# Kernel optimization log

Hardware: AMD Instinct MI355X
Metric: run time of the kernel (lower is better)

## Reference

```python
import jax, jax.numpy as jnp
import numpy as np

LN_EPS = 1e-12


def setup_inputs() -> dict:
    key = jax.random.key(0)
    k1, k2, k3, k4 = jax.random.split(key, 4)
    B, H, L, D = 2, 12, 2048, 64
    q = jax.random.normal(k1, (B, H, L, D), dtype=jnp.float32)
    k = jax.random.normal(k2, (B, H, L, D), dtype=jnp.float32)
    v = jax.random.normal(k3, (B, H, L, D), dtype=jnp.float32)
    mask = jax.random.randint(k4, (1, 1, L, L), 0, 2).astype(jnp.int32)
    gamma = jnp.ones((D,), dtype=jnp.float32)
    beta = jnp.zeros((D,), dtype=jnp.float32)
    return {"q": q, "k": k, "v": v, "mask": mask, "gamma": gamma, "beta": beta}


def reference(q, k, v, mask, gamma, beta):
    # score = q @ k^T  -> [B, H, L, L]
    score = jnp.einsum("bhqd,bhkd->bhqk", q, k)
    # masked_fill(mask == 0, -10000)
    score = jnp.where(mask == 0, jnp.float32(-10000.0), score)
    # result = score @ v -> [B, H, L, D]  (no softmax)
    result = jnp.einsum("bhqk,bhkd->bhqd", score, v)
    # layer norm over the last dim (d_tensor)
    mean = jnp.mean(result, axis=-1, keepdims=True)
    var = jnp.var(result, axis=-1, keepdims=True)
    normed = (result - mean) / jnp.sqrt(var + LN_EPS)
    return normed * gamma + beta
```

## Files before the change

kernel.cpp:

```cpp
#include <hip/hip_runtime.h>

#define SEQ 2048
#define HD 64
#define NBH 24
#define ROWB 144

#define MB_OFF   0
#define MB_BYTES (32 * 32 * 512)
#define QB_OFF   (MB_OFF + MB_BYTES)
#define QK_BYTES (NBH * SEQ * HD * 2)
#define KB_OFF   (QB_OFF + QK_BYTES)
#define VT_OFF   (KB_OFF + QK_BYTES)
#define WS_NEED  ((size_t)(VT_OFF + QK_BYTES))

typedef __bf16 bfrag8 __attribute__((ext_vector_type(8)));
typedef __bf16 bf16x4 __attribute__((ext_vector_type(4)));
typedef float  floatx4 __attribute__((ext_vector_type(4)));

__device__ __forceinline__ floatx4 mfma_16x16x32(bfrag8 a, bfrag8 b, floatx4 c) {
    return __builtin_amdgcn_mfma_f32_16x16x32_bf16(a, b, c, 0, 0, 0);
}

__global__ __launch_bounds__(256)
void prep_kernel(const float* __restrict__ qp, const float* __restrict__ kp,
                 const float* __restrict__ vp, const int* __restrict__ maskp,
                 unsigned char* __restrict__ ws)
{
    __shared__ __attribute__((aligned(16))) unsigned char parena[64 * 68 * 4];
    const int t = threadIdx.x;
    const int b = blockIdx.x;

    if (b < 1536) {
        int gt  = b * 256 + t;
        int row = gt >> 3;
        int c   = gt & 7;
        const floatx4* qs = (const floatx4*)(qp + row * 64 + c * 8);
        const floatx4* ks = (const floatx4*)(kp + row * 64 + c * 8);
        floatx4 q0 = qs[0], q1 = qs[1];
        floatx4 k0 = ks[0], k1 = ks[1];
        bfrag8 qpk, kpk;
        #pragma unroll
        for (int i = 0; i < 4; ++i) {
            qpk[i] = (__bf16)q0[i]; qpk[4 + i] = (__bf16)q1[i];
            kpk[i] = (__bf16)k0[i]; kpk[4 + i] = (__bf16)k1[i];
        }
        *(bfrag8*)(ws + QB_OFF + row * 128 + c * 16) = qpk;
        *(bfrag8*)(ws + KB_OFF + row * 128 + c * 16) = kpk;
    } else if (b < 2304) {
        int bb = b - 1536, bh = bb >> 5, kt = bb & 31;
        float* lf = (float*)parena;
        const floatx4* vg = (const floatx4*)(vp + (bh * SEQ + kt * 64) * 64);
        #pragma unroll
        for (int it = 0; it < 4; ++it) {
            int f = t + it * 256;
            int r = f >> 4, c4 = f & 15;
            floatx4 val = vg[f];
            #pragma unroll
            for (int i = 0; i < 4; ++i) lf[r * 68 + c4 * 4 + i] = val[i];
        }
        __syncthreads();
        int d = t >> 2, kseg = t & 3;
        unsigned char* tb = ws + VT_OFF + (size_t)(bh * 32 + kt) * 8192 + d * 128;
        #pragma unroll
        for (int jj = 0; jj < 2; ++jj) {
            bfrag8 pk;
            #pragma unroll
            for (int e = 0; e < 8; ++e)
                pk[e] = (__bf16)lf[(kseg * 16 + jj * 8 + e) * 68 + d];
            *(bfrag8*)(tb + (kseg * 2 + jj) * 16) = pk;
        }
    } else {
        int cc = b - 2304, qtb = cc >> 5, kt = cc & 31;
        const int w = t >> 6, lane = t & 63;
        #pragma unroll
        for (int it = 0; it < 16; ++it) {
            int rr = it * 4 + w;
            unsigned long long bl = __ballot(maskp[(qtb * 64 + rr) * SEQ + kt * 64 + lane] != 0);
            if (lane == 0)
                *(unsigned long long*)(ws + MB_OFF + (size_t)((qtb * 32 + kt) * 64 + rr) * 8) = bl;
        }
    }
}

__global__ __launch_bounds__(256, 3)
void normattn_main(const unsigned char* __restrict__ ws,
                   const float* __restrict__ gammap, const float* __restrict__ betap,
                   float* __restrict__ outp)
{
    __shared__ __attribute__((aligned(16))) unsigned char sK[2][64 * ROWB];
    __shared__ __attribute__((aligned(16))) unsigned char sV[2][64 * ROWB];
    __shared__ __attribute__((aligned(16))) unsigned char sS[64 * ROWB];

    const int tid  = threadIdx.x;
    const int w    = tid >> 6;
    const int lane = tid & 63;
    const int quad = lane >> 4;
    const int l16  = lane & 15;
    const int qtb  = blockIdx.x;
    const int bh   = blockIdx.y;
    const int q0   = qtb * 64;

    const unsigned char* gKb = ws + KB_OFF + (size_t)(bh * SEQ) * 128;
    const unsigned char* gVb = ws + VT_OFF + (size_t)(bh * 32) * 8192;
    const unsigned char* gMb = ws + MB_OFF + (size_t)(qtb * 32) * 512;

    bfrag8 qb[4][2];
    #pragma unroll
    for (int qt = 0; qt < 4; ++qt) {
        const unsigned char* gQ = ws + QB_OFF + (size_t)(bh * SEQ + q0 + qt * 16 + l16) * 128 + quad * 16;
        qb[qt][0] = *(const bfrag8*)gQ;
        qb[qt][1] = *(const bfrag8*)(gQ + 64);
    }

    floatx4 acc[4];
    #pragma unroll
    for (int i = 0; i < 4; ++i) acc[i] = (floatx4)0.0f;
    const int qrow_loc = w * 16 + quad * 4;

    const int sr0 = tid >> 3, sc0 = tid & 7;
    const int sr1 = (tid + 256) >> 3, sc1 = tid & 7;

    auto load_tile = [&](int kt, bfrag8 (&kr)[2], bfrag8 (&vr)[2]) {
        const unsigned char* gK = gKb + (size_t)kt * 8192;
        const unsigned char* gV = gVb + (size_t)kt * 8192;
        kr[0] = *(const bfrag8*)(gK + tid * 16);
        kr[1] = *(const bfrag8*)(gK + (tid + 256) * 16);
        vr[0] = *(const bfrag8*)(gV + tid * 16);
        vr[1] = *(const bfrag8*)(gV + (tid + 256) * 16);
    };
    auto write_tile = [&](int p, bfrag8 (&kr)[2], bfrag8 (&vr)[2]) {
        *(bfrag8*)(&sK[p][0] + sr0 * ROWB + sc0 * 16) = kr[0];
        *(bfrag8*)(&sK[p][0] + sr1 * ROWB + sc1 * 16) = kr[1];
        *(bfrag8*)(&sV[p][0] + sr0 * ROWB + sc0 * 16) = vr[0];
        *(bfrag8*)(&sV[p][0] + sr1 * ROWB + sc1 * 16) = vr[1];
    };

    {
        bfrag8 kr[2], vr[2];
        load_tile(0, kr, vr);
        write_tile(0, kr, vr);
    }
    unsigned long long mr[4];
    #pragma unroll
    for (int qt = 0; qt < 4; ++qt)
        mr[qt] = *(const unsigned long long*)(gMb + (qt * 16 + l16) * 8);
    __syncthreads();

    for (int kt = 0; kt < 32; ++kt) {
        const int p = kt & 1;

        bfrag8 kr[2], vr[2];
        if (kt < 31) load_tile(kt + 1, kr, vr);
        const int ktn = (kt < 31) ? kt + 1 : 31;
        unsigned long long mrn[4];
        #pragma unroll
        for (int qt = 0; qt < 4; ++qt)
            mrn[qt] = *(const unsigned long long*)(gMb + (size_t)ktn * 512 + (qt * 16 + l16) * 8);

        const unsigned char* cK = &sK[p][0];
        const unsigned char* cV = &sV[p][0];

        bfrag8 ka0 = *(const bfrag8*)(cK + (w * 16 + l16) * ROWB + quad * 16);
        bfrag8 ka1 = *(const bfrag8*)(cK + (w * 16 + l16) * ROWB + 64 + quad * 16);

        #pragma unroll
        for (int qt = 0; qt < 4; ++qt) {
            floatx4 st = (floatx4)0.0f;
            st = mfma_16x16x32(ka0, qb[qt][0], st);
            st = mfma_16x16x32(ka1, qb[qt][1], st);
            unsigned long long m4 = mr[qt] >> (w * 16 + quad * 4);
            bf16x4 pk;
            #pragma unroll
            for (int r = 0; r < 4; ++r) {
                float v = ((m4 >> r) & 1ull) ? st[r] : -10000.0f;
                pk[r] = (__bf16)v;
            }
            *(bf16x4*)(sS + (qt * 16 + l16) * ROWB + w * 32 + quad * 8) = pk;
        }
        asm volatile("s_waitcnt lgkmcnt(0)" ::: "memory");
        asm volatile("s_barrier" ::: "memory");

        #pragma unroll
        for (int kc2 = 0; kc2 < 2; ++kc2) {
            bfrag8 pa = *(const bfrag8*)(sS + (w * 16 + l16) * ROWB + kc2 * 64 + quad * 16);
            #pragma unroll
            for (int nt = 0; nt < 4; ++nt) {
                bfrag8 vb = *(const bfrag8*)(cV + (nt * 16 + l16) * ROWB + kc2 * 64 + quad * 16);
                acc[nt] = mfma_16x16x32(pa, vb, acc[nt]);
            }
        }

        if (kt < 31) write_tile(p ^ 1, kr, vr);
        asm volatile("s_waitcnt lgkmcnt(0)" ::: "memory");
        asm volatile("s_barrier" ::: "memory");

        #pragma unroll
        for (int qt = 0; qt < 4; ++qt) mr[qt] = mrn[qt];
    }

    float g[4], bt[4];
    #pragma unroll
    for (int nt = 0; nt < 4; ++nt) {
        g[nt]  = gammap[nt * 16 + l16];
        bt[nt] = betap[nt * 16 + l16];
    }
    #pragma unroll
    for (int r = 0; r < 4; ++r) {
        float s = 0.0f, s2 = 0.0f;
        #pragma unroll
        for (int nt = 0; nt < 4; ++nt) { float x = acc[nt][r]; s += x; s2 += x * x; }
        #pragma unroll
        for (int off = 1; off < 16; off <<= 1) {
            s  += __shfl_xor(s, off);
            s2 += __shfl_xor(s2, off);
        }
        float mean = s * (1.0f / 64.0f);
        float var  = s2 * (1.0f / 64.0f) - mean * mean;
        float rstd = rsqrtf(var + 1e-12f);
        float* orow = outp + (size_t)(bh * SEQ + q0 + qrow_loc + r) * 64;
        #pragma unroll
        for (int nt = 0; nt < 4; ++nt)
            orow[nt * 16 + l16] = (acc[nt][r] - mean) * rstd * g[nt] + bt[nt];
    }
}

#define KROW 72
#define SROW 40
__global__ __launch_bounds__(256, 4)
void normattn_fallback(const float* __restrict__ qp, const float* __restrict__ kp,
                       const float* __restrict__ vp, const int* __restrict__ maskp,
                       const float* __restrict__ gammap, const float* __restrict__ betap,
                       float* __restrict__ outp)
{
    __shared__ __attribute__((aligned(16))) __bf16 sQ[64 * KROW];
    __shared__ __attribute__((aligned(16))) __bf16 sK[64 * KROW];
    __shared__ __attribute__((aligned(16))) __bf16 sV[64 * KROW];
    __shared__ __attribute__((aligned(16))) __bf16 sS[4][16 * SROW];
    __shared__ __attribute__((aligned(8)))  unsigned int sMw[64][2];

    const int tid = threadIdx.x, wave = tid >> 6, lane = tid & 63;
    const int quad = lane >> 4, l16 = lane & 15;
    const int q0 = blockIdx.x * 64, bh = blockIdx.y;
    const int base = bh * SEQ * HD;
    {
        const floatx4* qg = (const floatx4*)(qp + base + q0 * HD);
        #pragma unroll
        for (int it = 0; it < 4; ++it) {
            int idx = tid + it * 256, r = idx >> 4, c = idx & 15;
            floatx4 val = qg[idx];
            bf16x4 pk = {(__bf16)val[0], (__bf16)val[1], (__bf16)val[2], (__bf16)val[3]};
            *(bf16x4*)&sQ[r * KROW + c * 4] = pk;
        }
    }
    __syncthreads();
    bfrag8 qa0 = *(const bfrag8*)&sQ[(wave * 16 + l16) * KROW + quad * 8];
    bfrag8 qa1 = *(const bfrag8*)&sQ[(wave * 16 + l16) * KROW + quad * 8 + 32];
    floatx4 acc[4];
    #pragma unroll
    for (int i = 0; i < 4; ++i) acc[i] = (floatx4)0.0f;
    const int qrow_loc = wave * 16 + quad * 4;
    const int qrb = q0 + qrow_loc;
    for (int kb = 0; kb < SEQ; kb += 64) {
        __syncthreads();
        {
            const floatx4* kg = (const floatx4*)(kp + base + kb * HD);
            #pragma unroll
            for (int it = 0; it < 4; ++it) {
                int idx = tid + it * 256, r = idx >> 4, c = idx & 15;
                floatx4 val = kg[idx];
                bf16x4 pk = {(__bf16)val[0], (__bf16)val[1], (__bf16)val[2], (__bf16)val[3]};
                *(bf16x4*)&sK[r * KROW + c * 4] = pk;
            }
        }
        {
            int d = tid & 63;
            #pragma unroll
            for (int it = 0; it < 4; ++it) {
                int k4 = (tid >> 6) + it * 4;
                bf16x4 pk;
                #pragma unroll
                for (int i = 0; i < 4; ++i) pk[i] = (__bf16)vp[base + (kb + k4 * 4 + i) * HD + d];
                *(bf16x4*)&sV[d * KROW + k4 * 4] = pk;
            }
        }
        #pragma unroll
        for (int it = 0; it < 16; ++it) {
            int rr = it * 4 + wave;
            unsigned long long bl = __ballot(maskp[(q0 + rr) * SEQ + kb + lane] != 0);
            if (lane == 0) { sMw[rr][0] = (unsigned)bl; sMw[rr][1] = (unsigned)(bl >> 32); }
        }
        __syncthreads();
        unsigned long long mrow[4];
        #pragma unroll
        for (int r = 0; r < 4; ++r) mrow[r] = *(const unsigned long long*)&sMw[qrow_loc + r][0];
        #pragma unroll
        for (int kc = 0; kc < 64; kc += 32) {
            floatx4 s0 = (floatx4)0.0f, s1 = (floatx4)0.0f;
            bfrag8 b00 = *(const bfrag8*)&sK[(kc + l16) * KROW + quad * 8];
            bfrag8 b01 = *(const bfrag8*)&sK[(kc + l16) * KROW + quad * 8 + 32];
            bfrag8 b10 = *(const bfrag8*)&sK[(kc + 16 + l16) * KROW + quad * 8];
            bfrag8 b11 = *(const bfrag8*)&sK[(kc + 16 + l16) * KROW + quad * 8 + 32];
            s0 = mfma_16x16x32(qa0, b00, s0);
            s0 = mfma_16x16x32(qa1, b01, s0);
            s1 = mfma_16x16x32(qa0, b10, s1);
            s1 = mfma_16x16x32(qa1, b11, s1);
            #pragma unroll
            for (int r = 0; r < 4; ++r) {
                float v0 = ((mrow[r] >> (kc + l16)) & 1ull) ? s0[r] : -10000.0f;
                float v1 = ((mrow[r] >> (kc + 16 + l16)) & 1ull) ? s1[r] : -10000.0f;
                sS[wave][(quad * 4 + r) * SROW + l16] = (__bf16)v0;
                sS[wave][(quad * 4 + r) * SROW + 16 + l16] = (__bf16)v1;
            }
            asm volatile("s_waitcnt lgkmcnt(0)" ::: "memory");
            bfrag8 pa = *(const bfrag8*)&sS[wave][l16 * SROW + quad * 8];
            #pragma unroll
            for (int nt = 0; nt < 4; ++nt) {
                bfrag8 vb = *(const bfrag8*)&sV[(nt * 16 + l16) * KROW + kc + quad * 8];
                acc[nt] = mfma_16x16x32(pa, vb, acc[nt]);
            }
        }
    }
    float g[4], bt[4];
    #pragma unroll
    for (int nt = 0; nt < 4; ++nt) { g[nt] = gammap[nt * 16 + l16]; bt[nt] = betap[nt * 16 + l16]; }
    #pragma unroll
    for (int r = 0; r < 4; ++r) {
        float s = 0.0f, s2 = 0.0f;
        #pragma unroll
        for (int nt = 0; nt < 4; ++nt) { float xx = acc[nt][r]; s += xx; s2 += xx * xx; }
        #pragma unroll
        for (int off = 1; off < 16; off <<= 1) { s += __shfl_xor(s, off); s2 += __shfl_xor(s2, off); }
        float mean = s * (1.0f / 64.0f);
        float var = s2 * (1.0f / 64.0f) - mean * mean;
        float rstd = rsqrtf(var + 1e-12f);
        float* orow = outp + base + (qrb + r) * HD;
        #pragma unroll
        for (int nt = 0; nt < 4; ++nt)
            orow[nt * 16 + l16] = (acc[nt][r] - mean) * rstd * g[nt] + bt[nt];
    }
}

extern "C" void kernel_launch(void* const* d_in, const int* in_sizes, int n_in,
                              void* d_out, int out_size, void* d_ws, size_t ws_size,
                              hipStream_t stream) {
    const float* q     = (const float*)d_in[0];
    const float* k     = (const float*)d_in[1];
    const float* v     = (const float*)d_in[2];
    const int*   mask  = (const int*)d_in[3];
    const float* gamma = (const float*)d_in[4];
    const float* beta  = (const float*)d_in[5];
    float* out = (float*)d_out;

    dim3 grid(32, NBH);
    if (ws_size >= WS_NEED) {
        unsigned char* ws = (unsigned char*)d_ws;
        prep_kernel<<<3328, 256, 0, stream>>>(q, k, v, mask, ws);
        normattn_main<<<grid, 256, 0, stream>>>(ws, gamma, beta, out);
    } else {
        normattn_fallback<<<grid, 256, 0, stream>>>(q, k, v, mask, gamma, beta, out);
    }
}
```

Baseline: 151.4 us.

## Process two key tiles per iteration and XOR-swizzle the score buffer

```diff
diff --git a/kernel.cpp b/kernel.cpp
--- a/kernel.cpp
+++ b/kernel.cpp
@@ -89,7 +89,7 @@
 {
     __shared__ __attribute__((aligned(16))) unsigned char sK[2][64 * ROWB];
     __shared__ __attribute__((aligned(16))) unsigned char sV[2][64 * ROWB];
-    __shared__ __attribute__((aligned(16))) unsigned char sS[64 * ROWB];
+    __shared__ __attribute__((aligned(16))) unsigned char sS[2][64 * 128];
 
     const int tid  = threadIdx.x;
     const int w    = tid >> 6;
@@ -99,6 +99,7 @@
     const int qtb  = blockIdx.x;
     const int bh   = blockIdx.y;
     const int q0   = qtb * 64;
+    const int swz  = l16 & 7;
 
     const unsigned char* gKb = ws + KB_OFF + (size_t)(bh * SEQ) * 128;
     const unsigned char* gVb = ws + VT_OFF + (size_t)(bh * 32) * 8192;
@@ -128,41 +129,16 @@
         vr[0] = *(const bfrag8*)(gV + tid * 16);
         vr[1] = *(const bfrag8*)(gV + (tid + 256) * 16);
     };
-    auto write_tile = [&](int p, bfrag8 (&kr)[2], bfrag8 (&vr)[2]) {
-        *(bfrag8*)(&sK[p][0] + sr0 * ROWB + sc0 * 16) = kr[0];
-        *(bfrag8*)(&sK[p][0] + sr1 * ROWB + sc1 * 16) = kr[1];
-        *(bfrag8*)(&sV[p][0] + sr0 * ROWB + sc0 * 16) = vr[0];
-        *(bfrag8*)(&sV[p][0] + sr1 * ROWB + sc1 * 16) = vr[1];
+    auto write_tile = [&](int s, bfrag8 (&kr)[2], bfrag8 (&vr)[2]) {
+        *(bfrag8*)(&sK[s][0] + sr0 * ROWB + sc0 * 16) = kr[0];
+        *(bfrag8*)(&sK[s][0] + sr1 * ROWB + sc1 * 16) = kr[1];
+        *(bfrag8*)(&sV[s][0] + sr0 * ROWB + sc0 * 16) = vr[0];
+        *(bfrag8*)(&sV[s][0] + sr1 * ROWB + sc1 * 16) = vr[1];
     };
 
-    {
-        bfrag8 kr[2], vr[2];
-        load_tile(0, kr, vr);
-        write_tile(0, kr, vr);
-    }
-    unsigned long long mr[4];
-    #pragma unroll
-    for (int qt = 0; qt < 4; ++qt)
-        mr[qt] = *(const unsigned long long*)(gMb + (qt * 16 + l16) * 8);
-    __syncthreads();
-
-    for (int kt = 0; kt < 32; ++kt) {
-        const int p = kt & 1;
-
-        bfrag8 kr[2], vr[2];
-        if (kt < 31) load_tile(kt + 1, kr, vr);
-        const int ktn = (kt < 31) ? kt + 1 : 31;
-        unsigned long long mrn[4];
-        #pragma unroll
-        for (int qt = 0; qt < 4; ++qt)
-            mrn[qt] = *(const unsigned long long*)(gMb + (size_t)ktn * 512 + (qt * 16 + l16) * 8);
-
-        const unsigned char* cK = &sK[p][0];
-        const unsigned char* cV = &sV[p][0];
-
+    auto qk_phase = [&](int tt, const unsigned char* cK, const unsigned long long (&mr)[4]) {
         bfrag8 ka0 = *(const bfrag8*)(cK + (w * 16 + l16) * ROWB + quad * 16);
         bfrag8 ka1 = *(const bfrag8*)(cK + (w * 16 + l16) * ROWB + 64 + quad * 16);
-
         #pragma unroll
         for (int qt = 0; qt < 4; ++qt) {
             floatx4 st = (floatx4)0.0f;
@@ -175,27 +151,65 @@
                 float v = ((m4 >> r) & 1ull) ? st[r] : -10000.0f;
                 pk[r] = (__bf16)v;
             }
-            *(bf16x4*)(sS + (qt * 16 + l16) * ROWB + w * 32 + quad * 8) = pk;
-        }
-        asm volatile("s_waitcnt lgkmcnt(0)" ::: "memory");
-        asm volatile("s_barrier" ::: "memory");
-
+            *(bf16x4*)(&sS[tt][0] + (qt * 16 + l16) * 128 +
+                       (((w * 2 + (quad >> 1)) ^ swz) * 16) + (quad & 1) * 8) = pk;
+        }
+    };
+    auto pv_phase = [&](int tt, const unsigned char* cV) {
         #pragma unroll
         for (int kc2 = 0; kc2 < 2; ++kc2) {
-            bfrag8 pa = *(const bfrag8*)(sS + (w * 16 + l16) * ROWB + kc2 * 64 + quad * 16);
+            bfrag8 pa = *(const bfrag8*)(&sS[tt][0] + (w * 16 + l16) * 128 +
+                                         (((kc2 * 4 + quad) ^ swz) * 16));
             #pragma unroll
             for (int nt = 0; nt < 4; ++nt) {
                 bfrag8 vb = *(const bfrag8*)(cV + (nt * 16 + l16) * ROWB + kc2 * 64 + quad * 16);
                 acc[nt] = mfma_16x16x32(pa, vb, acc[nt]);
             }
         }
-
-        if (kt < 31) write_tile(p ^ 1, kr, vr);
+    };
+
+    {
+        bfrag8 k0r[2], v0r[2], k1r[2], v1r[2];
+        load_tile(0, k0r, v0r);
+        load_tile(1, k1r, v1r);
+        write_tile(0, k0r, v0r);
+        write_tile(1, k1r, v1r);
+    }
+    asm volatile("s_waitcnt lgkmcnt(0)" ::: "memory");
+    asm volatile("s_barrier" ::: "memory");
+
+    for (int i = 0; i < 16; ++i) {
+        const int t0 = 2 * i, t1 = 2 * i + 1;
+
+        bfrag8 kA[2], vA[2];
+        if (i < 15) load_tile(t0 + 2, kA, vA);
+
+        unsigned long long mr0[4], mr1[4];
+        #pragma unroll
+        for (int qt = 0; qt < 4; ++qt) {
+            mr0[qt] = *(const unsigned long long*)(gMb + (size_t)t0 * 512 + (qt * 16 + l16) * 8);
+            mr1[qt] = *(const unsigned long long*)(gMb + (size_t)t1 * 512 + (qt * 16 + l16) * 8);
+        }
+
+        qk_phase(0, &sK[0][0], mr0);
+        qk_phase(1, &sK[1][0], mr1);
         asm volatile("s_waitcnt lgkmcnt(0)" ::: "memory");
         asm volatile("s_barrier" ::: "memory");
 
-        #pragma unroll
-        for (int qt = 0; qt < 4; ++qt) mr[qt] = mrn[qt];
+        bfrag8 kB[2], vB[2];
+        if (i < 15) load_tile(t0 + 3, kB, vB);
+
+        pv_phase(0, &sV[0][0]);
+        pv_phase(1, &sV[1][0]);
+        asm volatile("s_waitcnt lgkmcnt(0)" ::: "memory");
+        asm volatile("s_barrier" ::: "memory");
+
+        if (i < 15) {
+            write_tile(0, kA, vA);
+            write_tile(1, kB, vB);
+        }
+        asm volatile("s_waitcnt lgkmcnt(0)" ::: "memory");
+        asm volatile("s_barrier" ::: "memory");
     }
 
     float g[4], bt[4];
```

Result: faster. 147.7 us (-2.4%).
